# Kernel optimization log

Hardware: AMD Instinct MI355X
Metric: run time of the kernel (lower is better)

Reference implementation:

```python
import jax, jax.numpy as jnp
import numpy as np

TOP_K = 2
NORM_TOPK = True


def setup_inputs() -> dict:
    key = jax.random.key(0)
    k1, k2, k3, k4 = jax.random.split(key, 4)
    B, S, H = 2, 1024, 2048
    E, I = 16, 768
    hidden_states = jax.random.normal(k1, (B, S, H), dtype=jnp.float32)
    gate_w = jax.random.normal(k2, (E, H), dtype=jnp.float32) * 0.02
    gate_up_w = jax.random.normal(k3, (E, 2 * I, H), dtype=jnp.float32) * 0.02
    down_w = jax.random.normal(k4, (E, H, I), dtype=jnp.float32) * 0.02
    return {
        "hidden_states": hidden_states,
        "gate_w": gate_w,
        "gate_up_w": gate_up_w,
        "down_w": down_w,
        "top_k": TOP_K,
    }


def reference(hidden_states, gate_w, gate_up_w, down_w, top_k):
    B, S, H = hidden_states.shape
    E = gate_w.shape[0]
    x = hidden_states.reshape(-1, H)  # [T, H]
    T = x.shape[0]

    # Router: softmax in float32 (as in torch F.softmax(..., dtype=torch.float))
    router_logits = x @ gate_w.T  # [T, E]
    probs = jax.nn.softmax(router_logits.astype(jnp.float32), axis=-1)
    top_w, top_idx = jax.lax.top_k(probs, top_k)  # [T, k]
    if NORM_TOPK:
        top_w = top_w / jnp.sum(top_w, axis=-1, keepdims=True)
    top_w = top_w.astype(x.dtype)

    # Dense combine weights [T, E]: routing weight where selected, 0 elsewhere.
    comb = jnp.sum(jax.nn.one_hot(top_idx, E, dtype=x.dtype) * top_w[..., None], axis=1)

    # SwiGLU expert MLPs evaluated for all experts, combined with sparse weights.
    gu = jnp.einsum("th,efh->tef", x, gate_up_w)  # [T, E, 2I]
    g, u = jnp.split(gu, 2, axis=-1)
    h = jax.nn.silu(g) * u  # [T, E, I]
    y = jnp.einsum("tei,ehi->teh", h, down_w)  # [T, E, H]
    out = jnp.einsum("teh,te->th", y, comb)  # [T, H]

    return out.reshape(B, S, H), router_logits
```

## Files before the change

### kernel.cpp

```cpp
#include <hip/hip_runtime.h>
#include <hip/hip_bf16.h>

#define T_TOK 2048
#define H_DIM 2048
#define E_NUM 16
#define I_DIM 768

typedef __bf16 bf16;
typedef __bf16 bf16x4 __attribute__((ext_vector_type(4)));
typedef __bf16 bf16x8 __attribute__((ext_vector_type(8)));
typedef float f32x4 __attribute__((ext_vector_type(4)));

__global__ __launch_bounds__(256) void router_kernel(
    const float* __restrict__ x, const float* __restrict__ gw,
    float* __restrict__ logits, int* __restrict__ cnt,
    int* __restrict__ tok_list, float* __restrict__ wgt_list)
{
    int t = blockIdx.x;
    int tid = threadIdx.x;
    __shared__ double red[E_NUM][256];
    double part[E_NUM];
#pragma unroll
    for (int e = 0; e < E_NUM; ++e) part[e] = 0.0;
    for (int h = tid; h < H_DIM; h += 256) {
        double xv = (double)x[(size_t)t * H_DIM + h];
#pragma unroll
        for (int e = 0; e < E_NUM; ++e)
            part[e] += xv * (double)gw[e * H_DIM + h];
    }
#pragma unroll
    for (int e = 0; e < E_NUM; ++e) red[e][tid] = part[e];
    __syncthreads();
    for (int s = 128; s > 0; s >>= 1) {
        if (tid < s) {
#pragma unroll
            for (int e = 0; e < E_NUM; ++e) red[e][tid] += red[e][tid + s];
        }
        __syncthreads();
    }
    __shared__ float lg[E_NUM];
    if (tid < E_NUM) {
        float v = (float)red[tid][0];
        lg[tid] = v;
        logits[(size_t)t * E_NUM + tid] = v;
    }
    __syncthreads();
    if (tid == 0) {
        int i0 = 0; float v0 = lg[0];
#pragma unroll
        for (int e = 1; e < E_NUM; ++e) if (lg[e] > v0) { v0 = lg[e]; i0 = e; }
        int i1 = -1; float v1 = -3.4e38f;
#pragma unroll
        for (int e = 0; e < E_NUM; ++e) if (e != i0 && lg[e] > v1) { v1 = lg[e]; i1 = e; }
        float w0 = 1.0f / (1.0f + __expf(v1 - v0));
        float w1 = 1.0f - w0;
        int p0 = atomicAdd(&cnt[i0], 1);
        tok_list[i0 * T_TOK + p0] = t; wgt_list[i0 * T_TOK + p0] = w0;
        int p1 = atomicAdd(&cnt[i1], 1);
        tok_list[i1 * T_TOK + p1] = t; wgt_list[i1 * T_TOK + p1] = w1;
    }
}

__global__ void scan_kernel(const int* __restrict__ cnt, int* __restrict__ offs)
{
    if (threadIdx.x == 0) {
        int o = 0;
        for (int e = 0; e < E_NUM; ++e) { offs[e] = o; o += cnt[e]; }
    }
}

#define TM 128
#define BK 64
#define LDK 72

__global__ __launch_bounds__(256) void gateup_kernel(
    const float* __restrict__ x, const float* __restrict__ gup,
    const int* __restrict__ cnt, const int* __restrict__ offs,
    const int* __restrict__ tok_list, bf16* __restrict__ hbuf)
{
    int e = blockIdx.z;
    int count = cnt[e];
    int row0 = blockIdx.y * TM;
    if (row0 >= count) return;
    int i0 = blockIdx.x * 64;
    const float* W = gup + (size_t)e * (2 * I_DIM) * H_DIM;
    int hoff = offs[e];

    __shared__ __align__(16) bf16 As[TM][LDK];
    __shared__ __align__(16) bf16 Bs[128][LDK];
    __shared__ int toks[TM];

    int tid = threadIdx.x;
    if (tid < TM) {
        int r = row0 + tid;
        if (r > count - 1) r = count - 1;
        toks[tid] = tok_list[e * T_TOK + r];
    }
    __syncthreads();

    int lane = tid & 63, wid = tid >> 6;
    int wm = wid >> 1, wn = wid & 1;
    int la = lane & 15, lq = lane >> 4;

    f32x4 accg[4][2], accu[4][2];
#pragma unroll
    for (int a = 0; a < 4; ++a)
#pragma unroll
        for (int b = 0; b < 2; ++b) {
            accg[a][b] = (f32x4){0.f, 0.f, 0.f, 0.f};
            accu[a][b] = (f32x4){0.f, 0.f, 0.f, 0.f};
        }

    int ar = tid >> 1;
    int ac = (tid & 1) * 32;
    const float* xrow = x + (size_t)toks[ar] * H_DIM;
    int brow = (ar < 64) ? (i0 + ar) : (768 + i0 + (ar - 64));
    const float* wrow = W + (size_t)brow * H_DIM;

    for (int k0 = 0; k0 < H_DIM; k0 += BK) {
#pragma unroll
        for (int j = 0; j < 8; ++j) {
            float4 v = *(const float4*)(xrow + k0 + ac + 4 * j);
            bf16x4 b = { (bf16)v.x, (bf16)v.y, (bf16)v.z, (bf16)v.w };
            *(bf16x4*)&As[ar][ac + 4 * j] = b;
        }
#pragma unroll
        for (int j = 0; j < 8; ++j) {
            float4 v = *(const float4*)(wrow + k0 + ac + 4 * j);
            bf16x4 b = { (bf16)v.x, (bf16)v.y, (bf16)v.z, (bf16)v.w };
            *(bf16x4*)&Bs[ar][ac + 4 * j] = b;
        }
        __syncthreads();
#pragma unroll
        for (int ks = 0; ks < BK; ks += 32) {
            bf16x8 af[4], bg[2], bu[2];
#pragma unroll
            for (int mt = 0; mt < 4; ++mt)
                af[mt] = *(const bf16x8*)&As[64 * wm + 16 * mt + la][ks + lq * 8];
#pragma unroll
            for (int nt = 0; nt < 2; ++nt) {
                bg[nt] = *(const bf16x8*)&Bs[32 * wn + 16 * nt + la][ks + lq * 8];
                bu[nt] = *(const bf16x8*)&Bs[64 + 32 * wn + 16 * nt + la][ks + lq * 8];
            }
#pragma unroll
            for (int mt = 0; mt < 4; ++mt)
#pragma unroll
                for (int nt = 0; nt < 2; ++nt) {
                    accg[mt][nt] = __builtin_amdgcn_mfma_f32_16x16x32_bf16(af[mt], bg[nt], accg[mt][nt], 0, 0, 0);
                    accu[mt][nt] = __builtin_amdgcn_mfma_f32_16x16x32_bf16(af[mt], bu[nt], accu[mt][nt], 0, 0, 0);
                }
        }
        __syncthreads();
    }
#pragma unroll
    for (int mt = 0; mt < 4; ++mt)
#pragma unroll
        for (int nt = 0; nt < 2; ++nt)
#pragma unroll
            for (int r = 0; r < 4; ++r) {
                int lrow = 64 * wm + 16 * mt + lq * 4 + r;
                if (row0 + lrow < count) {
                    int col = i0 + 32 * wn + 16 * nt + la;
                    float g = accg[mt][nt][r], u = accu[mt][nt][r];
                    float hv = (g / (1.0f + __expf(-g))) * u;
                    hbuf[(size_t)(hoff + row0 + lrow) * I_DIM + col] = (bf16)hv;
                }
            }
}

__global__ __launch_bounds__(256) void down_kernel(
    const float* __restrict__ dw, const bf16* __restrict__ hbuf,
    const int* __restrict__ cnt, const int* __restrict__ offs,
    const int* __restrict__ tok_list, const float* __restrict__ wgt_list,
    float* __restrict__ out)
{
    int e = blockIdx.z;
    int count = cnt[e];
    int row0 = blockIdx.y * TM;
    if (row0 >= count) return;
    int n0 = blockIdx.x * 128;
    const float* W = dw + (size_t)e * H_DIM * I_DIM;
    int hoff = offs[e];

    __shared__ __align__(16) bf16 As[TM][LDK];
    __shared__ __align__(16) bf16 Bs[128][LDK];
    __shared__ int toks[TM];
    __shared__ float wgts[TM];

    int tid = threadIdx.x;
    if (tid < TM) {
        int r = row0 + tid;
        if (r > count - 1) r = count - 1;
        toks[tid] = tok_list[e * T_TOK + r];
        wgts[tid] = wgt_list[e * T_TOK + r];
    }
    __syncthreads();

    int lane = tid & 63, wid = tid >> 6;
    int wm = wid >> 1, wn = wid & 1;
    int la = lane & 15, lq = lane >> 4;

    f32x4 acc[4][4];
#pragma unroll
    for (int a = 0; a < 4; ++a)
#pragma unroll
        for (int b = 0; b < 4; ++b) acc[a][b] = (f32x4){0.f, 0.f, 0.f, 0.f};

    int ar = tid >> 1;
    int ac = (tid & 1) * 32;
    int arow = row0 + ar; if (arow > count - 1) arow = count - 1;
    const bf16* hrow = hbuf + (size_t)(hoff + arow) * I_DIM;
    const float* wrow = W + (size_t)(n0 + ar) * I_DIM;

    for (int k0 = 0; k0 < I_DIM; k0 += BK) {
#pragma unroll
        for (int j = 0; j < 4; ++j) {
            bf16x8 v = *(const bf16x8*)(hrow + k0 + ac + 8 * j);
            *(bf16x8*)&As[ar][ac + 8 * j] = v;
        }
#pragma unroll
        for (int j = 0; j < 8; ++j) {
            float4 v = *(const float4*)(wrow + k0 + ac + 4 * j);
            bf16x4 b = { (bf16)v.x, (bf16)v.y, (bf16)v.z, (bf16)v.w };
            *(bf16x4*)&Bs[ar][ac + 4 * j] = b;
        }
        __syncthreads();
#pragma unroll
        for (int ks = 0; ks < BK; ks += 32) {
            bf16x8 af[4], bb[4];
#pragma unroll
            for (int mt = 0; mt < 4; ++mt)
                af[mt] = *(const bf16x8*)&As[64 * wm + 16 * mt + la][ks + lq * 8];
#pragma unroll
            for (int nt = 0; nt < 4; ++nt)
                bb[nt] = *(const bf16x8*)&Bs[64 * wn + 16 * nt + la][ks + lq * 8];
#pragma unroll
            for (int mt = 0; mt < 4; ++mt)
#pragma unroll
                for (int nt = 0; nt < 4; ++nt)
                    acc[mt][nt] = __builtin_amdgcn_mfma_f32_16x16x32_bf16(af[mt], bb[nt], acc[mt][nt], 0, 0, 0);
        }
        __syncthreads();
    }
#pragma unroll
    for (int mt = 0; mt < 4; ++mt)
#pragma unroll
        for (int nt = 0; nt < 4; ++nt)
#pragma unroll
            for (int r = 0; r < 4; ++r) {
                int lrow = 64 * wm + 16 * mt + lq * 4 + r;
                if (row0 + lrow < count) {
                    int col = n0 + 64 * wn + 16 * nt + la;
                    atomicAdd(&out[(size_t)toks[lrow] * H_DIM + col],
                              wgts[lrow] * acc[mt][nt][r]);
                }
            }
}

extern "C" void kernel_launch(void* const* d_in, const int* in_sizes, int n_in,
                              void* d_out, int out_size, void* d_ws, size_t ws_size,
                              hipStream_t stream)
{
    const float* x   = (const float*)d_in[0];
    const float* gw  = (const float*)d_in[1];
    const float* gup = (const float*)d_in[2];
    const float* dw  = (const float*)d_in[3];
    float* out = (float*)d_out;
    float* logits = out + (size_t)T_TOK * H_DIM;

    char* ws = (char*)d_ws;
    int*   cnt      = (int*)(ws + 0);
    int*   offs     = (int*)(ws + 128);
    int*   tok_list = (int*)(ws + 256);
    float* wgt_list = (float*)(ws + 256 + 131072);
    bf16*  hbuf     = (bf16*)(ws + 256 + 262144);

    hipMemsetAsync(cnt, 0, 128, stream);
    hipMemsetAsync(out, 0, (size_t)T_TOK * H_DIM * sizeof(float), stream);

    router_kernel<<<T_TOK, 256, 0, stream>>>(x, gw, logits, cnt, tok_list, wgt_list);
    scan_kernel<<<1, 64, 0, stream>>>(cnt, offs);
    gateup_kernel<<<dim3(I_DIM / 64, T_TOK / TM, E_NUM), 256, 0, stream>>>(
        x, gup, cnt, offs, tok_list, hbuf);
    down_kernel<<<dim3(H_DIM / 128, T_TOK / TM, E_NUM), 256, 0, stream>>>(
        dw, hbuf, cnt, offs, tok_list, wgt_list, out);
}
```

Baseline: 653.2 us.

## Pre-convert weights and activations to bf16 and use async global-to-LDS loads

Adds a convert kernel that casts gate_up and down weights to bf16 once per call, and has the router also write a bf16 copy of x. The expert GEMMs then load bf16 tiles straight into XOR-swizzled LDS through global_load_lds. Row tiles shrink from 128 to 64 and launch bounds request 4 blocks per CU. This removes repeated fp32 loads and per-tile conversions across row blocks, in exchange for an extra full pass over roughly 200 MB of fp32 weights on every call.

```diff
diff --git a/kernel.cpp b/kernel.cpp
--- a/kernel.cpp
+++ b/kernel.cpp
@@ -1,5 +1,6 @@
 #include <hip/hip_runtime.h>
 #include <hip/hip_bf16.h>
+#include <stdint.h>
 
 #define T_TOK 2048
 #define H_DIM 2048
@@ -7,14 +8,20 @@
 #define I_DIM 768
 
 typedef __bf16 bf16;
-typedef __bf16 bf16x4 __attribute__((ext_vector_type(4)));
 typedef __bf16 bf16x8 __attribute__((ext_vector_type(8)));
 typedef float f32x4 __attribute__((ext_vector_type(4)));
+
+__device__ __forceinline__ void async_cp16(bf16* l, const bf16* g) {
+    __builtin_amdgcn_global_load_lds(
+        (const __attribute__((address_space(1))) void*)g,
+        (__attribute__((address_space(3))) void*)l, 16, 0, 0);
+}
 
 __global__ __launch_bounds__(256) void router_kernel(
     const float* __restrict__ x, const float* __restrict__ gw,
     float* __restrict__ logits, int* __restrict__ cnt,
-    int* __restrict__ tok_list, float* __restrict__ wgt_list)
+    int* __restrict__ tok_list, float* __restrict__ wgt_list,
+    bf16* __restrict__ xb)
 {
     int t = blockIdx.x;
     int tid = threadIdx.x;
@@ -23,7 +30,9 @@
 #pragma unroll
     for (int e = 0; e < E_NUM; ++e) part[e] = 0.0;
     for (int h = tid; h < H_DIM; h += 256) {
-        double xv = (double)x[(size_t)t * H_DIM + h];
+        float xf = x[(size_t)t * H_DIM + h];
+        xb[(size_t)t * H_DIM + h] = (bf16)xf;
+        double xv = (double)xf;
 #pragma unroll
         for (int e = 0; e < E_NUM; ++e)
             part[e] += xv * (double)gw[e * H_DIM + h];
@@ -69,190 +78,226 @@
     }
 }
 
-#define TM 128
-#define BK 64
-#define LDK 72
-
-__global__ __launch_bounds__(256) void gateup_kernel(
-    const float* __restrict__ x, const float* __restrict__ gup,
+__global__ __launch_bounds__(256) void convert_kernel(
+    const float* __restrict__ gup, const float* __restrict__ dwn,
+    bf16* __restrict__ gub, bf16* __restrict__ dwb)
+{
+    const size_t NG = (size_t)E_NUM * 2 * I_DIM * H_DIM / 8;
+    const size_t ND = (size_t)E_NUM * H_DIM * I_DIM / 8;
+    size_t stride = (size_t)gridDim.x * 256;
+    for (size_t c = (size_t)blockIdx.x * 256 + threadIdx.x; c < NG + ND; c += stride) {
+        const float* s; bf16* d; size_t off;
+        if (c < NG) { s = gup; d = gub; off = c * 8; }
+        else        { s = dwn; d = dwb; off = (c - NG) * 8; }
+        float4 a = *(const float4*)(s + off);
+        float4 b = *(const float4*)(s + off + 4);
+        bf16x8 v = { (bf16)a.x, (bf16)a.y, (bf16)a.z, (bf16)a.w,
+                     (bf16)b.x, (bf16)b.y, (bf16)b.z, (bf16)b.w };
+        *(bf16x8*)(d + off) = v;
+    }
+}
+
+__global__ __launch_bounds__(256, 4) void gateup_kernel(
+    const bf16* __restrict__ xb, const bf16* __restrict__ gub,
     const int* __restrict__ cnt, const int* __restrict__ offs,
     const int* __restrict__ tok_list, bf16* __restrict__ hbuf)
 {
-    int e = blockIdx.z;
-    int count = cnt[e];
-    int row0 = blockIdx.y * TM;
+    const int e = blockIdx.z;
+    const int count = cnt[e];
+    const int row0 = blockIdx.y * 64;
     if (row0 >= count) return;
-    int i0 = blockIdx.x * 64;
-    const float* W = gup + (size_t)e * (2 * I_DIM) * H_DIM;
-    int hoff = offs[e];
-
-    __shared__ __align__(16) bf16 As[TM][LDK];
-    __shared__ __align__(16) bf16 Bs[128][LDK];
-    __shared__ int toks[TM];
-
-    int tid = threadIdx.x;
-    if (tid < TM) {
-        int r = row0 + tid;
-        if (r > count - 1) r = count - 1;
+    const int i0 = blockIdx.x * 64;
+    const int hoff = offs[e];
+    const int tid = threadIdx.x;
+
+    __shared__ __align__(16) bf16 As[64 * 64];
+    __shared__ __align__(16) bf16 Bs[128 * 64];
+    __shared__ int toks[64];
+
+    if (tid < 64) {
+        int r = row0 + tid; if (r >= count) r = count - 1;
         toks[tid] = tok_list[e * T_TOK + r];
     }
     __syncthreads();
 
-    int lane = tid & 63, wid = tid >> 6;
-    int wm = wid >> 1, wn = wid & 1;
-    int la = lane & 15, lq = lane >> 4;
-
-    f32x4 accg[4][2], accu[4][2];
-#pragma unroll
-    for (int a = 0; a < 4; ++a)
-#pragma unroll
-        for (int b = 0; b < 2; ++b) {
-            accg[a][b] = (f32x4){0.f, 0.f, 0.f, 0.f};
-            accu[a][b] = (f32x4){0.f, 0.f, 0.f, 0.f};
+    const int lane = tid & 63, wid = tid >> 6;
+    const int la = lane & 15, lq = lane >> 4;
+    const int wm = wid >> 1, wn = wid & 1;
+
+    int ra0 = tid >> 3, s0 = tid & 7;
+    int ca0 = s0 ^ (ra0 & 7);
+    int ra1 = ra0 + 32;
+    int ca1 = s0 ^ (ra1 & 7);
+    const bf16* srcA0 = xb + (size_t)toks[ra0] * H_DIM + ca0 * 8;
+    const bf16* srcA1 = xb + (size_t)toks[ra1] * H_DIM + ca1 * 8;
+    bf16* dstA0 = As + (size_t)(wid * 64) * 8;
+    bf16* dstA1 = As + (size_t)(wid * 64 + 256) * 8;
+
+    const bf16* srcB[4]; bf16* dstB[4];
+#pragma unroll
+    for (int i = 0; i < 4; ++i) {
+        int idx = tid + 256 * i;
+        int r = idx >> 3, s = idx & 7;
+        int c8 = s ^ (r & 7);
+        int is_u = (r >> 5) & 1;
+        int ioff = (r >> 6) * 32 + (r & 31);
+        size_t grow = (size_t)e * (2 * I_DIM) + (size_t)is_u * I_DIM + i0 + ioff;
+        srcB[i] = gub + grow * H_DIM + c8 * 8;
+        dstB[i] = Bs + (size_t)(256 * i + wid * 64) * 8;
+    }
+
+    f32x4 acc[2][4];
+#pragma unroll
+    for (int a = 0; a < 2; ++a)
+#pragma unroll
+        for (int b = 0; b < 4; ++b) acc[a][b] = (f32x4){0.f, 0.f, 0.f, 0.f};
+
+    for (int k0 = 0; k0 < H_DIM; k0 += 64) {
+        async_cp16(dstA0, srcA0 + k0);
+        async_cp16(dstA1, srcA1 + k0);
+#pragma unroll
+        for (int i = 0; i < 4; ++i) async_cp16(dstB[i], srcB[i] + k0);
+        __syncthreads();
+#pragma unroll
+        for (int ks = 0; ks < 2; ++ks) {
+            bf16x8 af[2], bfr[4];
+            int ch = lq + 4 * ks;
+#pragma unroll
+            for (int mt = 0; mt < 2; ++mt) {
+                int row = 32 * wm + 16 * mt + la;
+                int sl = ch ^ (row & 7);
+                af[mt] = *(const bf16x8*)(As + (size_t)(row * 8 + sl) * 8);
+            }
+#pragma unroll
+            for (int nt = 0; nt < 4; ++nt) {
+                int row = 64 * wn + 16 * nt + la;
+                int sl = ch ^ (row & 7);
+                bfr[nt] = *(const bf16x8*)(Bs + (size_t)(row * 8 + sl) * 8);
+            }
+#pragma unroll
+            for (int mt = 0; mt < 2; ++mt)
+#pragma unroll
+                for (int nt = 0; nt < 4; ++nt)
+                    acc[mt][nt] = __builtin_amdgcn_mfma_f32_16x16x32_bf16(af[mt], bfr[nt], acc[mt][nt], 0, 0, 0);
         }
-
-    int ar = tid >> 1;
-    int ac = (tid & 1) * 32;
-    const float* xrow = x + (size_t)toks[ar] * H_DIM;
-    int brow = (ar < 64) ? (i0 + ar) : (768 + i0 + (ar - 64));
-    const float* wrow = W + (size_t)brow * H_DIM;
-
-    for (int k0 = 0; k0 < H_DIM; k0 += BK) {
-#pragma unroll
-        for (int j = 0; j < 8; ++j) {
-            float4 v = *(const float4*)(xrow + k0 + ac + 4 * j);
-            bf16x4 b = { (bf16)v.x, (bf16)v.y, (bf16)v.z, (bf16)v.w };
-            *(bf16x4*)&As[ar][ac + 4 * j] = b;
-        }
-#pragma unroll
-        for (int j = 0; j < 8; ++j) {
-            float4 v = *(const float4*)(wrow + k0 + ac + 4 * j);
-            bf16x4 b = { (bf16)v.x, (bf16)v.y, (bf16)v.z, (bf16)v.w };
-            *(bf16x4*)&Bs[ar][ac + 4 * j] = b;
-        }
-        __syncthreads();
-#pragma unroll
-        for (int ks = 0; ks < BK; ks += 32) {
-            bf16x8 af[4], bg[2], bu[2];
-#pragma unroll
-            for (int mt = 0; mt < 4; ++mt)
-                af[mt] = *(const bf16x8*)&As[64 * wm + 16 * mt + la][ks + lq * 8];
-#pragma unroll
-            for (int nt = 0; nt < 2; ++nt) {
-                bg[nt] = *(const bf16x8*)&Bs[32 * wn + 16 * nt + la][ks + lq * 8];
-                bu[nt] = *(const bf16x8*)&Bs[64 + 32 * wn + 16 * nt + la][ks + lq * 8];
-            }
-#pragma unroll
-            for (int mt = 0; mt < 4; ++mt)
-#pragma unroll
-                for (int nt = 0; nt < 2; ++nt) {
-                    accg[mt][nt] = __builtin_amdgcn_mfma_f32_16x16x32_bf16(af[mt], bg[nt], accg[mt][nt], 0, 0, 0);
-                    accu[mt][nt] = __builtin_amdgcn_mfma_f32_16x16x32_bf16(af[mt], bu[nt], accu[mt][nt], 0, 0, 0);
+        __syncthreads();
+    }
+
+#pragma unroll
+    for (int mt = 0; mt < 2; ++mt)
+#pragma unroll
+        for (int p = 0; p < 2; ++p)
+#pragma unroll
+            for (int r = 0; r < 4; ++r) {
+                int trow = 32 * wm + 16 * mt + lq * 4 + r;
+                if (row0 + trow < count) {
+                    float g = acc[mt][p][r], u = acc[mt][p + 2][r];
+                    float hv = (g / (1.0f + __expf(-g))) * u;
+                    int col = i0 + 32 * wn + 16 * p + la;
+                    hbuf[(size_t)(hoff + row0 + trow) * I_DIM + col] = (bf16)hv;
                 }
-        }
-        __syncthreads();
-    }
-#pragma unroll
-    for (int mt = 0; mt < 4; ++mt)
-#pragma unroll
-        for (int nt = 0; nt < 2; ++nt)
-#pragma unroll
-            for (int r = 0; r < 4; ++r) {
-                int lrow = 64 * wm + 16 * mt + lq * 4 + r;
-                if (row0 + lrow < count) {
-                    int col = i0 + 32 * wn + 16 * nt + la;
-                    float g = accg[mt][nt][r], u = accu[mt][nt][r];
-                    float hv = (g / (1.0f + __expf(-g))) * u;
-                    hbuf[(size_t)(hoff + row0 + lrow) * I_DIM + col] = (bf16)hv;
-                }
-            }
-}
-
-__global__ __launch_bounds__(256) void down_kernel(
-    const float* __restrict__ dw, const bf16* __restrict__ hbuf,
+            }
+}
+
+__global__ __launch_bounds__(256, 4) void down_kernel(
+    const bf16* __restrict__ dwb, const bf16* __restrict__ hbuf,
     const int* __restrict__ cnt, const int* __restrict__ offs,
     const int* __restrict__ tok_list, const float* __restrict__ wgt_list,
     float* __restrict__ out)
 {
-    int e = blockIdx.z;
-    int count = cnt[e];
-    int row0 = blockIdx.y * TM;
+    const int e = blockIdx.z;
+    const int count = cnt[e];
+    const int row0 = blockIdx.y * 64;
     if (row0 >= count) return;
-    int n0 = blockIdx.x * 128;
-    const float* W = dw + (size_t)e * H_DIM * I_DIM;
-    int hoff = offs[e];
-
-    __shared__ __align__(16) bf16 As[TM][LDK];
-    __shared__ __align__(16) bf16 Bs[128][LDK];
-    __shared__ int toks[TM];
-    __shared__ float wgts[TM];
-
-    int tid = threadIdx.x;
-    if (tid < TM) {
-        int r = row0 + tid;
-        if (r > count - 1) r = count - 1;
+    const int n0 = blockIdx.x * 128;
+    const int hoff = offs[e];
+    const int tid = threadIdx.x;
+
+    __shared__ __align__(16) bf16 As[64 * 64];
+    __shared__ __align__(16) bf16 Bs[128 * 64];
+    __shared__ int toks[64];
+    __shared__ float wgts[64];
+
+    if (tid < 64) {
+        int r = row0 + tid; if (r >= count) r = count - 1;
         toks[tid] = tok_list[e * T_TOK + r];
         wgts[tid] = wgt_list[e * T_TOK + r];
     }
     __syncthreads();
 
-    int lane = tid & 63, wid = tid >> 6;
-    int wm = wid >> 1, wn = wid & 1;
-    int la = lane & 15, lq = lane >> 4;
-
-    f32x4 acc[4][4];
-#pragma unroll
-    for (int a = 0; a < 4; ++a)
+    const int lane = tid & 63, wid = tid >> 6;
+    const int la = lane & 15, lq = lane >> 4;
+    const int wm = wid >> 1, wn = wid & 1;
+
+    int ra0 = tid >> 3, s0 = tid & 7;
+    int ca0 = s0 ^ (ra0 & 7);
+    int ra1 = ra0 + 32;
+    int ca1 = s0 ^ (ra1 & 7);
+    int ar0 = row0 + ra0; if (ar0 >= count) ar0 = count - 1;
+    int ar1 = row0 + ra1; if (ar1 >= count) ar1 = count - 1;
+    const bf16* srcA0 = hbuf + (size_t)(hoff + ar0) * I_DIM + ca0 * 8;
+    const bf16* srcA1 = hbuf + (size_t)(hoff + ar1) * I_DIM + ca1 * 8;
+    bf16* dstA0 = As + (size_t)(wid * 64) * 8;
+    bf16* dstA1 = As + (size_t)(wid * 64 + 256) * 8;
+
+    const bf16* srcB[4]; bf16* dstB[4];
+#pragma unroll
+    for (int i = 0; i < 4; ++i) {
+        int idx = tid + 256 * i;
+        int r = idx >> 3, s = idx & 7;
+        int c8 = s ^ (r & 7);
+        srcB[i] = dwb + ((size_t)e * H_DIM + n0 + r) * I_DIM + c8 * 8;
+        dstB[i] = Bs + (size_t)(256 * i + wid * 64) * 8;
+    }
+
+    f32x4 acc[2][4];
+#pragma unroll
+    for (int a = 0; a < 2; ++a)
 #pragma unroll
         for (int b = 0; b < 4; ++b) acc[a][b] = (f32x4){0.f, 0.f, 0.f, 0.f};
 
-    int ar = tid >> 1;
-    int ac = (tid & 1) * 32;
-    int arow = row0 + ar; if (arow > count - 1) arow = count - 1;
-    const bf16* hrow = hbuf + (size_t)(hoff + arow) * I_DIM;
-    const float* wrow = W + (size_t)(n0 + ar) * I_DIM;
-
-    for (int k0 = 0; k0 < I_DIM; k0 += BK) {
-#pragma unroll
-        for (int j = 0; j < 4; ++j) {
-            bf16x8 v = *(const bf16x8*)(hrow + k0 + ac + 8 * j);
-            *(bf16x8*)&As[ar][ac + 8 * j] = v;
+    for (int k0 = 0; k0 < I_DIM; k0 += 64) {
+        async_cp16(dstA0, srcA0 + k0);
+        async_cp16(dstA1, srcA1 + k0);
+#pragma unroll
+        for (int i = 0; i < 4; ++i) async_cp16(dstB[i], srcB[i] + k0);
+        __syncthreads();
+#pragma unroll
+        for (int ks = 0; ks < 2; ++ks) {
+            bf16x8 af[2], bfr[4];
+            int ch = lq + 4 * ks;
+#pragma unroll
+            for (int mt = 0; mt < 2; ++mt) {
+                int row = 32 * wm + 16 * mt + la;
+                int sl = ch ^ (row & 7);
+                af[mt] = *(const bf16x8*)(As + (size_t)(row * 8 + sl) * 8);
+            }
+#pragma unroll
+            for (int nt = 0; nt < 4; ++nt) {
+                int row = 64 * wn + 16 * nt + la;
+                int sl = ch ^ (row & 7);
+                bfr[nt] = *(const bf16x8*)(Bs + (size_t)(row * 8 + sl) * 8);
+            }
+#pragma unroll
+            for (int mt = 0; mt < 2; ++mt)
+#pragma unroll
+                for (int nt = 0; nt < 4; ++nt)
+                    acc[mt][nt] = __builtin_amdgcn_mfma_f32_16x16x32_bf16(af[mt], bfr[nt], acc[mt][nt], 0, 0, 0);
         }
-#pragma unroll
-        for (int j = 0; j < 8; ++j) {
-            float4 v = *(const float4*)(wrow + k0 + ac + 4 * j);
-            bf16x4 b = { (bf16)v.x, (bf16)v.y, (bf16)v.z, (bf16)v.w };
-            *(bf16x4*)&Bs[ar][ac + 4 * j] = b;
-        }
-        __syncthreads();
-#pragma unroll
-        for (int ks = 0; ks < BK; ks += 32) {
-            bf16x8 af[4], bb[4];
-#pragma unroll
-            for (int mt = 0; mt < 4; ++mt)
-                af[mt] = *(const bf16x8*)&As[64 * wm + 16 * mt + la][ks + lq * 8];
-#pragma unroll
-            for (int nt = 0; nt < 4; ++nt)
-                bb[nt] = *(const bf16x8*)&Bs[64 * wn + 16 * nt + la][ks + lq * 8];
-#pragma unroll
-            for (int mt = 0; mt < 4; ++mt)
-#pragma unroll
-                for (int nt = 0; nt < 4; ++nt)
-                    acc[mt][nt] = __builtin_amdgcn_mfma_f32_16x16x32_bf16(af[mt], bb[nt], acc[mt][nt], 0, 0, 0);
-        }
-        __syncthreads();
-    }
-#pragma unroll
-    for (int mt = 0; mt < 4; ++mt)
+        __syncthreads();
+    }
+
+#pragma unroll
+    for (int mt = 0; mt < 2; ++mt)
 #pragma unroll
         for (int nt = 0; nt < 4; ++nt)
 #pragma unroll
             for (int r = 0; r < 4; ++r) {
-                int lrow = 64 * wm + 16 * mt + lq * 4 + r;
-                if (row0 + lrow < count) {
+                int trow = 32 * wm + 16 * mt + lq * 4 + r;
+                if (row0 + trow < count) {
                     int col = n0 + 64 * wn + 16 * nt + la;
-                    atomicAdd(&out[(size_t)toks[lrow] * H_DIM + col],
-                              wgts[lrow] * acc[mt][nt][r]);
+                    atomicAdd(&out[(size_t)toks[trow] * H_DIM + col],
+                              wgts[trow] * acc[mt][nt][r]);
                 }
             }
 }
@@ -270,18 +315,22 @@
 
     char* ws = (char*)d_ws;
     int*   cnt      = (int*)(ws + 0);
-    int*   offs     = (int*)(ws + 128);
-    int*   tok_list = (int*)(ws + 256);
-    float* wgt_list = (float*)(ws + 256 + 131072);
-    bf16*  hbuf     = (bf16*)(ws + 256 + 262144);
-
-    hipMemsetAsync(cnt, 0, 128, stream);
+    int*   offs     = (int*)(ws + 256);
+    int*   tok_list = (int*)(ws + 512);
+    float* wgt_list = (float*)(ws + 131584);
+    bf16*  hbuf     = (bf16*)(ws + 262656);
+    bf16*  xb       = (bf16*)(ws + 6554112);
+    bf16*  gub      = (bf16*)(ws + 14942720);
+    bf16*  dwb      = (bf16*)(ws + 115606016);
+
+    hipMemsetAsync(cnt, 0, 256, stream);
     hipMemsetAsync(out, 0, (size_t)T_TOK * H_DIM * sizeof(float), stream);
 
-    router_kernel<<<T_TOK, 256, 0, stream>>>(x, gw, logits, cnt, tok_list, wgt_list);
+    convert_kernel<<<4096, 256, 0, stream>>>(gup, dw, gub, dwb);
+    router_kernel<<<T_TOK, 256, 0, stream>>>(x, gw, logits, cnt, tok_list, wgt_list, xb);
     scan_kernel<<<1, 64, 0, stream>>>(cnt, offs);
-    gateup_kernel<<<dim3(I_DIM / 64, T_TOK / TM, E_NUM), 256, 0, stream>>>(
-        x, gup, cnt, offs, tok_list, hbuf);
-    down_kernel<<<dim3(H_DIM / 128, T_TOK / TM, E_NUM), 256, 0, stream>>>(
-        dw, hbuf, cnt, offs, tok_list, wgt_list, out);
-}
+    gateup_kernel<<<dim3(I_DIM / 64, T_TOK / 64, E_NUM), 256, 0, stream>>>(
+        xb, gub, cnt, offs, tok_list, hbuf);
+    down_kernel<<<dim3(H_DIM / 128, T_TOK / 64, E_NUM), 256, 0, stream>>>(
+        dwb, hbuf, cnt, offs, tok_list, wgt_list, out);
+}
```

Result: faster. 555.5 us (-15.0%).
